# Performance work log

Measured on AMD Instinct MI355X. Metric: run time of the kernel, lower is better.

The kernel has to match this reference:

```python
import jax, jax.numpy as jnp
import numpy as np

B, C, H, W = 64, 3, 384, 384


def setup_inputs() -> dict:
    key = jax.random.key(0)
    k1, k2 = jax.random.split(key)
    imgs = jax.random.normal(k1, (B, C, H, W), dtype=jnp.float32)
    eye = jnp.broadcast_to(jnp.eye(2, 3, dtype=jnp.float32), (B, 2, 3))
    theta = eye + 0.05 * jax.random.normal(k2, (B, 2, 3), dtype=jnp.float32)
    return {"imgs": imgs, "theta": theta}


def _gen_affine_grid(theta, h, w):
    # Mirrors torchvision functional_tensor._gen_affine_grid (align_corners=False style).
    # theta: [2,3]; returns normalized grid [h, w, 2] in [-1, 1].
    d = 0.5
    xs = jnp.linspace(-w * 0.5 + d, w * 0.5 + d - 1, w, dtype=jnp.float32)  # [w]
    ys = jnp.linspace(-h * 0.5 + d, h * 0.5 + d - 1, h, dtype=jnp.float32)  # [h]
    # base_grid[y, x] = (xs[x], ys[y], 1)
    xg, yg = jnp.meshgrid(xs, ys)  # each [h, w]
    ones = jnp.ones_like(xg)
    base = jnp.stack([xg, yg, ones], axis=-1)  # [h, w, 3]
    scale = jnp.array([0.5 * w, 0.5 * h], dtype=jnp.float32)
    rescaled_theta = theta.T / scale  # [3, 2]
    return base @ rescaled_theta  # [h, w, 2]


def _grid_sample_bilinear(img, grid):
    # img: [C, H, W], grid: [H, W, 2] normalized coords, zeros padding,
    # align_corners=False (torch grid_sample semantics).
    c, h, w = img.shape
    ix = (grid[..., 0] + 1.0) * w * 0.5 - 0.5  # [H, W]
    iy = (grid[..., 1] + 1.0) * h * 0.5 - 0.5
    x0 = jnp.floor(ix)
    y0 = jnp.floor(iy)
    wx1 = ix - x0
    wy1 = iy - y0
    wx0 = 1.0 - wx1
    wy0 = 1.0 - wy1

    def gather(xi, yi):
        valid = (xi >= 0) & (xi < w) & (yi >= 0) & (yi < h)
        xc = jnp.clip(xi, 0, w - 1).astype(jnp.int32)
        yc = jnp.clip(yi, 0, h - 1).astype(jnp.int32)
        v = img[:, yc, xc]  # [C, H, W] gather
        return v * valid.astype(img.dtype)

    out = (gather(x0, y0) * (wx0 * wy0)
           + gather(x0 + 1, y0) * (wx1 * wy0)
           + gather(x0, y0 + 1) * (wx0 * wy1)
           + gather(x0 + 1, y0 + 1) * (wx1 * wy1))
    return out  # [C, H, W]


def reference(imgs, theta):
    b, c, h, w = imgs.shape

    def per_image(img, th):
        grid = _gen_affine_grid(th, h, w)
        return _grid_sample_bilinear(img, grid)

    return jax.vmap(per_image)(imgs, theta)  # [B, C, H, W]
```

## Files before the change

### kernel.cpp

```cpp
#include <hip/hip_runtime.h>

#define B_ 64
#define C_ 3
#define H_ 384
#define W_ 384
#define HW_ (H_ * W_)

typedef float f32x2 __attribute__((ext_vector_type(2)));
typedef f32x2 __attribute__((aligned(4))) f32x2_u;

__global__ __launch_bounds__(256) void affine_sample_kernel(
    const float* __restrict__ imgs,
    const float* __restrict__ theta,
    float* __restrict__ out)
{
    int nb = gridDim.x;
    int bid = blockIdx.x;
    int sb = (bid & 7) * (nb >> 3) + (bid >> 3);

    int b   = sb / 576;
    int rem = sb - b * 576;
    int rp  = rem / 3;
    int xt  = rem - rp * 3;

    int tid = threadIdx.x;
    int x = xt * 128 + (tid & 127);
    int y = rp * 2 + (tid >> 7);

    const float* th = theta + b * 6;
    float t00 = th[0], t01 = th[1], t02 = th[2];
    float t10 = th[3], t11 = th[4], t12 = th[5];

    float xg = (float)x - 191.5f;
    float yg = (float)y - 191.5f;

    float ix = fmaf(xg, t00, fmaf(yg, t01, t02)) + 191.5f;
    float iy = fmaf(xg, t10, fmaf(yg, t11, t12)) + 191.5f;

    float x0f = floorf(ix);
    float y0f = floorf(iy);
    float wx1 = ix - x0f;
    float wy1 = iy - y0f;
    float wx0 = 1.0f - wx1;
    float wy0 = 1.0f - wy1;
    float x1f = x0f + 1.0f;
    float y1f = y0f + 1.0f;

    bool vx0 = (x0f >= 0.0f) && (x0f < (float)W_);
    bool vx1 = (x1f >= 0.0f) && (x1f < (float)W_);
    bool vy0 = (y0f >= 0.0f) && (y0f < (float)H_);
    bool vy1 = (y1f >= 0.0f) && (y1f < (float)H_);

    int x0 = (int)fminf(fmaxf(x0f, 0.0f), (float)(W_ - 1));
    int x1 = (int)fminf(fmaxf(x1f, 0.0f), (float)(W_ - 1));
    int y0 = (int)fminf(fmaxf(y0f, 0.0f), (float)(H_ - 1));
    int y1 = (int)fminf(fmaxf(y1f, 0.0f), (float)(H_ - 1));

    int xb = (int)fminf(fmaxf(x0f, 0.0f), (float)(W_ - 2));

    bool selx0 = (x0 == xb);
    bool selx1 = (x1 == xb);

    float w00 = wx0 * wy0 * ((vx0 && vy0) ? 1.0f : 0.0f);
    float w01 = wx1 * wy0 * ((vx1 && vy0) ? 1.0f : 0.0f);
    float w10 = wx0 * wy1 * ((vx0 && vy1) ? 1.0f : 0.0f);
    float w11 = wx1 * wy1 * ((vx1 && vy1) ? 1.0f : 0.0f);

    int oT = y0 * W_ + xb;
    int oB = y1 * W_ + xb;

    const float* bimg = imgs + (size_t)b * (C_ * HW_);
    float* bout = out + (size_t)b * (C_ * HW_) + y * W_ + x;

    f32x2 vt[C_], vb[C_];
#pragma unroll
    for (int c = 0; c < C_; ++c) {
        const float* p = bimg + c * HW_;
        vt[c] = *reinterpret_cast<const f32x2_u*>(p + oT);
        vb[c] = *reinterpret_cast<const f32x2_u*>(p + oB);
    }

#pragma unroll
    for (int c = 0; c < C_; ++c) {
        float v00 = selx0 ? vt[c].x : vt[c].y;
        float v01 = selx1 ? vt[c].x : vt[c].y;
        float v10 = selx0 ? vb[c].x : vb[c].y;
        float v11 = selx1 ? vb[c].x : vb[c].y;
        float r = fmaf(v00, w00, fmaf(v01, w01,
                  fmaf(v10, w10, v11 * w11)));
        bout[c * HW_] = r;
    }
}

extern "C" void kernel_launch(void* const* d_in, const int* in_sizes, int n_in,
                              void* d_out, int out_size, void* d_ws, size_t ws_size,
                              hipStream_t stream) {
    const float* imgs = (const float*)d_in[0];
    const float* theta = (const float*)d_in[1];
    float* out = (float*)d_out;
    int total = B_ * H_ * W_;
    affine_sample_kernel<<<total / 256, 256, 0, stream>>>(imgs, theta, out);
}
```

Measured before the change: 208.7 us.

## Stage source footprint in LDS per 64x8 output tile for bilinear sampling

Measured after the change: 210.7 us. No clear change (+1.0%).

```diff
diff --git a/kernel.cpp b/kernel.cpp
--- a/kernel.cpp
+++ b/kernel.cpp
@@ -5,7 +5,15 @@
 #define H_ 384
 #define W_ 384
 #define HW_ (H_ * W_)
-
+#define TOTALF ((size_t)B_ * C_ * HW_)
+
+#define TW 64
+#define TH 8
+#define NRMAX 24
+#define NCMAX 84
+#define NWMAX 21
+
+typedef float f32x4 __attribute__((ext_vector_type(4)));
 typedef float f32x2 __attribute__((ext_vector_type(2)));
 typedef f32x2 __attribute__((aligned(4))) f32x2_u;
 
@@ -14,81 +22,197 @@
     const float* __restrict__ theta,
     float* __restrict__ out)
 {
+    __shared__ float smem[C_][NRMAX][NCMAX];
+
     int nb = gridDim.x;
     int bid = blockIdx.x;
     int sb = (bid & 7) * (nb >> 3) + (bid >> 3);
 
-    int b   = sb / 576;
-    int rem = sb - b * 576;
-    int rp  = rem / 3;
-    int xt  = rem - rp * 3;
-
-    int tid = threadIdx.x;
-    int x = xt * 128 + (tid & 127);
-    int y = rp * 2 + (tid >> 7);
+    int b   = sb / 288;
+    int rem = sb - b * 288;
+    int yt  = rem / 6;
+    int xt  = rem - yt * 6;
+    b = __builtin_amdgcn_readfirstlane(b);
 
     const float* th = theta + b * 6;
     float t00 = th[0], t01 = th[1], t02 = th[2];
     float t10 = th[3], t11 = th[4], t12 = th[5];
 
+    float xgl = (float)(xt * TW) - 191.5f;
+    float xgr = xgl + (float)(TW - 1);
+    float ygt = (float)(yt * TH) - 191.5f;
+    float ygb = ygt + (float)(TH - 1);
+
+    float ix00 = fmaf(xgl, t00, fmaf(ygt, t01, t02)) + 191.5f;
+    float ix10 = fmaf(xgr, t00, fmaf(ygt, t01, t02)) + 191.5f;
+    float ix01 = fmaf(xgl, t00, fmaf(ygb, t01, t02)) + 191.5f;
+    float ix11 = fmaf(xgr, t00, fmaf(ygb, t01, t02)) + 191.5f;
+    float iy00 = fmaf(xgl, t10, fmaf(ygt, t11, t12)) + 191.5f;
+    float iy10 = fmaf(xgr, t10, fmaf(ygt, t11, t12)) + 191.5f;
+    float iy01 = fmaf(xgl, t10, fmaf(ygb, t11, t12)) + 191.5f;
+    float iy11 = fmaf(xgr, t10, fmaf(ygb, t11, t12)) + 191.5f;
+
+    float ixmin = fminf(fminf(ix00, ix10), fminf(ix01, ix11)) - 0.01f;
+    float ixmax = fmaxf(fmaxf(ix00, ix10), fmaxf(ix01, ix11)) + 0.01f;
+    float iymin = fminf(fminf(iy00, iy10), fminf(iy01, iy11)) - 0.01f;
+    float iymax = fmaxf(fmaxf(iy00, iy10), fmaxf(iy01, iy11)) + 0.01f;
+
+    int cl  = (int)fminf(fmaxf(floorf(ixmin), 0.0f), (float)(W_ - 2));
+    int chp = (int)fminf(fmaxf(floorf(ixmax), 0.0f), (float)(W_ - 2)) + 1;
+    int rl  = (int)fminf(fmaxf(floorf(iymin), 0.0f), (float)(H_ - 1));
+    int rhi = (int)fminf(fmaxf(floorf(iymax) + 1.0f, 0.0f), (float)(H_ - 1));
+
+    int c0a = cl & ~3;
+    int NC  = chp - c0a + 1;
+    int NR  = rhi - rl + 1;
+
+    c0a = __builtin_amdgcn_readfirstlane(c0a);
+    rl  = __builtin_amdgcn_readfirstlane(rl);
+    NC  = __builtin_amdgcn_readfirstlane(NC);
+    NR  = __builtin_amdgcn_readfirstlane(NR);
+
+    bool accept = (NC <= NCMAX) && (NR <= NRMAX);
+
+    int tid = threadIdx.x;
+    int x = xt * TW + (tid & 63);
+    int y = yt * TH + ((tid >> 6) << 1);
+
+    const float* bimg = imgs + (size_t)b * (C_ * HW_);
+    float* boutbase = out + (size_t)b * (C_ * HW_) + (size_t)y * W_ + x;
+
     float xg = (float)x - 191.5f;
-    float yg = (float)y - 191.5f;
-
-    float ix = fmaf(xg, t00, fmaf(yg, t01, t02)) + 191.5f;
-    float iy = fmaf(xg, t10, fmaf(yg, t11, t12)) + 191.5f;
-
-    float x0f = floorf(ix);
-    float y0f = floorf(iy);
-    float wx1 = ix - x0f;
-    float wy1 = iy - y0f;
-    float wx0 = 1.0f - wx1;
-    float wy0 = 1.0f - wy1;
-    float x1f = x0f + 1.0f;
-    float y1f = y0f + 1.0f;
-
-    bool vx0 = (x0f >= 0.0f) && (x0f < (float)W_);
-    bool vx1 = (x1f >= 0.0f) && (x1f < (float)W_);
-    bool vy0 = (y0f >= 0.0f) && (y0f < (float)H_);
-    bool vy1 = (y1f >= 0.0f) && (y1f < (float)H_);
-
-    int x0 = (int)fminf(fmaxf(x0f, 0.0f), (float)(W_ - 1));
-    int x1 = (int)fminf(fmaxf(x1f, 0.0f), (float)(W_ - 1));
-    int y0 = (int)fminf(fmaxf(y0f, 0.0f), (float)(H_ - 1));
-    int y1 = (int)fminf(fmaxf(y1f, 0.0f), (float)(H_ - 1));
-
-    int xb = (int)fminf(fmaxf(x0f, 0.0f), (float)(W_ - 2));
-
-    bool selx0 = (x0 == xb);
-    bool selx1 = (x1 == xb);
-
-    float w00 = wx0 * wy0 * ((vx0 && vy0) ? 1.0f : 0.0f);
-    float w01 = wx1 * wy0 * ((vx1 && vy0) ? 1.0f : 0.0f);
-    float w10 = wx0 * wy1 * ((vx0 && vy1) ? 1.0f : 0.0f);
-    float w11 = wx1 * wy1 * ((vx1 && vy1) ? 1.0f : 0.0f);
-
-    int oT = y0 * W_ + xb;
-    int oB = y1 * W_ + xb;
-
-    const float* bimg = imgs + (size_t)b * (C_ * HW_);
-    float* bout = out + (size_t)b * (C_ * HW_) + y * W_ + x;
-
-    f32x2 vt[C_], vb[C_];
-#pragma unroll
-    for (int c = 0; c < C_; ++c) {
-        const float* p = bimg + c * HW_;
-        vt[c] = *reinterpret_cast<const f32x2_u*>(p + oT);
-        vb[c] = *reinterpret_cast<const f32x2_u*>(p + oB);
-    }
-
-#pragma unroll
-    for (int c = 0; c < C_; ++c) {
-        float v00 = selx0 ? vt[c].x : vt[c].y;
-        float v01 = selx1 ? vt[c].x : vt[c].y;
-        float v10 = selx0 ? vb[c].x : vb[c].y;
-        float v11 = selx1 ? vb[c].x : vb[c].y;
-        float r = fmaf(v00, w00, fmaf(v01, w01,
-                  fmaf(v10, w10, v11 * w11)));
-        bout[c * HW_] = r;
+
+    if (accept) {
+        int nw = (NC + 3) >> 2;
+#pragma unroll
+        for (int c = 0; c < C_; ++c) {
+#pragma unroll
+            for (int k = 0; k < 2; ++k) {
+                int idx  = tid + k * 256;
+                int row  = idx / NWMAX;
+                int col4 = idx - row * NWMAX;
+                if (row < NR && col4 < nw) {
+                    int gr = rl + row;
+                    int gc = c0a + col4 * 4;
+                    size_t goff = (size_t)b * (C_ * HW_) + (size_t)(c * HW_ + gr * W_ + gc);
+                    f32x4 vv;
+                    if (goff + 3 < TOTALF) {
+                        vv = *reinterpret_cast<const f32x4*>(imgs + goff);
+                    } else {
+                        vv.x = imgs[goff];
+                        vv.y = (goff + 1 < TOTALF) ? imgs[goff + 1] : 0.0f;
+                        vv.z = (goff + 2 < TOTALF) ? imgs[goff + 2] : 0.0f;
+                        vv.w = 0.0f;
+                    }
+                    *reinterpret_cast<f32x4*>(&smem[c][row][col4 * 4]) = vv;
+                }
+            }
+        }
+        __syncthreads();
+
+#pragma unroll
+        for (int pi = 0; pi < 2; ++pi) {
+            float yg = (float)(y + pi) - 191.5f;
+            float ix = fmaf(xg, t00, fmaf(yg, t01, t02)) + 191.5f;
+            float iy = fmaf(xg, t10, fmaf(yg, t11, t12)) + 191.5f;
+
+            float x0f = floorf(ix);
+            float y0f = floorf(iy);
+            float wx1 = ix - x0f;
+            float wy1 = iy - y0f;
+            float wx0 = 1.0f - wx1;
+            float wy0 = 1.0f - wy1;
+            float x1f = x0f + 1.0f;
+            float y1f = y0f + 1.0f;
+
+            bool vx0 = (x0f >= 0.0f) && (x0f < (float)W_);
+            bool vx1 = (x1f >= 0.0f) && (x1f < (float)W_);
+            bool vy0 = (y0f >= 0.0f) && (y0f < (float)H_);
+            bool vy1 = (y1f >= 0.0f) && (y1f < (float)H_);
+
+            int x0 = (int)fminf(fmaxf(x0f, 0.0f), (float)(W_ - 1));
+            int x1 = (int)fminf(fmaxf(x1f, 0.0f), (float)(W_ - 1));
+            int y0 = (int)fminf(fmaxf(y0f, 0.0f), (float)(H_ - 1));
+            int y1 = (int)fminf(fmaxf(y1f, 0.0f), (float)(H_ - 1));
+            int xb = (int)fminf(fmaxf(x0f, 0.0f), (float)(W_ - 2));
+
+            bool selx0 = (x0 == xb);
+            bool selx1 = (x1 == xb);
+
+            float w00 = wx0 * wy0 * ((vx0 && vy0) ? 1.0f : 0.0f);
+            float w01 = wx1 * wy0 * ((vx1 && vy0) ? 1.0f : 0.0f);
+            float w10 = wx0 * wy1 * ((vx0 && vy1) ? 1.0f : 0.0f);
+            float w11 = wx1 * wy1 * ((vx1 && vy1) ? 1.0f : 0.0f);
+
+            int lrT = y0 - rl;
+            int lrB = y1 - rl;
+            int lc  = xb - c0a;
+
+#pragma unroll
+            for (int c = 0; c < C_; ++c) {
+                float pTx = smem[c][lrT][lc], pTy = smem[c][lrT][lc + 1];
+                float pBx = smem[c][lrB][lc], pBy = smem[c][lrB][lc + 1];
+                float v00 = selx0 ? pTx : pTy;
+                float v01 = selx1 ? pTx : pTy;
+                float v10 = selx0 ? pBx : pBy;
+                float v11 = selx1 ? pBx : pBy;
+                float r = fmaf(v00, w00, fmaf(v01, w01,
+                          fmaf(v10, w10, v11 * w11)));
+                boutbase[c * HW_ + pi * W_] = r;
+            }
+        }
+    } else {
+#pragma unroll
+        for (int pi = 0; pi < 2; ++pi) {
+            float yg = (float)(y + pi) - 191.5f;
+            float ix = fmaf(xg, t00, fmaf(yg, t01, t02)) + 191.5f;
+            float iy = fmaf(xg, t10, fmaf(yg, t11, t12)) + 191.5f;
+
+            float x0f = floorf(ix);
+            float y0f = floorf(iy);
+            float wx1 = ix - x0f;
+            float wy1 = iy - y0f;
+            float wx0 = 1.0f - wx1;
+            float wy0 = 1.0f - wy1;
+            float x1f = x0f + 1.0f;
+            float y1f = y0f + 1.0f;
+
+            bool vx0 = (x0f >= 0.0f) && (x0f < (float)W_);
+            bool vx1 = (x1f >= 0.0f) && (x1f < (float)W_);
+            bool vy0 = (y0f >= 0.0f) && (y0f < (float)H_);
+            bool vy1 = (y1f >= 0.0f) && (y1f < (float)H_);
+
+            int x0 = (int)fminf(fmaxf(x0f, 0.0f), (float)(W_ - 1));
+            int x1 = (int)fminf(fmaxf(x1f, 0.0f), (float)(W_ - 1));
+            int y0 = (int)fminf(fmaxf(y0f, 0.0f), (float)(H_ - 1));
+            int y1 = (int)fminf(fmaxf(y1f, 0.0f), (float)(H_ - 1));
+            int xb = (int)fminf(fmaxf(x0f, 0.0f), (float)(W_ - 2));
+
+            bool selx0 = (x0 == xb);
+            bool selx1 = (x1 == xb);
+
+            float w00 = wx0 * wy0 * ((vx0 && vy0) ? 1.0f : 0.0f);
+            float w01 = wx1 * wy0 * ((vx1 && vy0) ? 1.0f : 0.0f);
+            float w10 = wx0 * wy1 * ((vx0 && vy1) ? 1.0f : 0.0f);
+            float w11 = wx1 * wy1 * ((vx1 && vy1) ? 1.0f : 0.0f);
+
+            int oT = y0 * W_ + xb;
+            int oB = y1 * W_ + xb;
+
+#pragma unroll
+            for (int c = 0; c < C_; ++c) {
+                const float* p = bimg + c * HW_;
+                f32x2 vt = *reinterpret_cast<const f32x2_u*>(p + oT);
+                f32x2 vb = *reinterpret_cast<const f32x2_u*>(p + oB);
+                float v00 = selx0 ? vt.x : vt.y;
+                float v01 = selx1 ? vt.x : vt.y;
+                float v10 = selx0 ? vb.x : vb.y;
+                float v11 = selx1 ? vb.x : vb.y;
+                float r = fmaf(v00, w00, fmaf(v01, w01,
+                          fmaf(v10, w10, v11 * w11)));
+                boutbase[c * HW_ + pi * W_] = r;
+            }
+        }
     }
 }
 
@@ -98,6 +222,6 @@
     const float* imgs = (const float*)d_in[0];
     const float* theta = (const float*)d_in[1];
     float* out = (float*)d_out;
-    int total = B_ * H_ * W_;
-    affine_sample_kernel<<<total / 256, 256, 0, stream>>>(imgs, theta, out);
+    int blocks = B_ * (H_ / TH) * (W_ / TW);
+    affine_sample_kernel<<<blocks, 256, 0, stream>>>(imgs, theta, out);
 }
```
